# Performance work log

Hardware: AMD Instinct MI355X
Metric: run time of the kernel (lower is better)

## Reference

```python
import math
import jax, jax.numpy as jnp
import numpy as np

H = 16          # num_attention_heads
DH = 64         # attention_head_size
D = H * DH      # hidden_size
MAX_POS = 1024  # max_position_embeddings


def setup_inputs() -> dict:
    key = jax.random.key(0)
    ks = jax.random.split(key, 9)
    B, S = 8, 1024
    scale = 0.02
    return {
        "hidden_states": jax.random.normal(ks[0], (B, S, D), dtype=jnp.float32),
        "attention_mask": jnp.zeros((B, 1, 1, S), dtype=jnp.float32),
        "Wq": jax.random.normal(ks[1], (D, D), dtype=jnp.float32) * scale,
        "bq": jnp.zeros((D,), dtype=jnp.float32),
        "Wk": jax.random.normal(ks[2], (D, D), dtype=jnp.float32) * scale,
        "bk": jnp.zeros((D,), dtype=jnp.float32),
        "Wv": jax.random.normal(ks[3], (D, D), dtype=jnp.float32) * scale,
        "bv": jnp.zeros((D,), dtype=jnp.float32),
        "dist_emb": jax.random.normal(ks[4], (2 * MAX_POS - 1, DH), dtype=jnp.float32) * scale,
    }


def reference(hidden_states, attention_mask, Wq, bq, Wk, bk, Wv, bv, dist_emb):
    B, S, _ = hidden_states.shape
    # projections -> [B, H, S, DH]
    def heads(x):
        return x.reshape(B, S, H, DH).transpose(0, 2, 1, 3)
    q = heads(hidden_states @ Wq + bq)
    k = heads(hidden_states @ Wk + bk)
    v = heads(hidden_states @ Wv + bv)

    # fp32_cast_query_key == 'manual': cast q,k to fp32 before matmul (already fp32 here)
    scores = jnp.einsum("bhld,bhrd->bhlr", q.astype(jnp.float32), k.astype(jnp.float32))
    scores = scores / math.sqrt(DH)

    # relative_key_query positional bias
    pos = jnp.arange(S)
    distance = pos[:, None] - pos[None, :] + (MAX_POS - 1)   # [S, S]
    pe = dist_emb[distance].astype(q.dtype)                   # [S, S, DH]
    scores = scores + jnp.einsum("bhld,lrd->bhlr", q, pe) \
                     + jnp.einsum("bhrd,lrd->bhlr", k, pe)

    scores = scores + attention_mask
    # fp32_cast_attention_scores=True: softmax in fp32
    probs = jax.nn.softmax(scores.astype(jnp.float32), axis=-1).astype(hidden_states.dtype)

    ctx = jnp.einsum("bhlr,bhrd->bhld", probs, v)  # [B, H, S, DH]
    ctx = ctx.transpose(0, 2, 1, 3).reshape(B, S, D)
    return ctx
```

## Files before the change

kernel.cpp:

```cpp
#include <hip/hip_runtime.h>
#include <stdint.h>

typedef unsigned short u16;
typedef short bf16x8 __attribute__((ext_vector_type(8)));
typedef float f32x4 __attribute__((ext_vector_type(4)));
typedef u16 u16x8 __attribute__((ext_vector_type(8)));
typedef u16 u16x4 __attribute__((ext_vector_type(4)));

#define NB 8
#define NS 1024
#define NH 16
#define NDH 64
#define ND 1024

#define AS1 __attribute__((address_space(1)))
#define AS3 __attribute__((address_space(3)))

__device__ __forceinline__ int SWZ(int row, int colbyte){
  return (row << 7) + (colbyte ^ ((row & 7) << 4));
}

__device__ __forceinline__ u16 f2b(float x){
  unsigned u = __float_as_uint(x);
  u += 0x7FFFu + ((u >> 16) & 1u);
  return (u16)(u >> 16);
}
__device__ __forceinline__ float b2f(u16 h){ return __uint_as_float(((unsigned)h) << 16); }

__global__ void cast_f32_bf16(const float* __restrict__ in, u16* __restrict__ out, long n){
  long i = ((long)blockIdx.x * blockDim.x + threadIdx.x) * 8;
  if (i + 8 <= n){
    float4 a = *(const float4*)&in[i];
    float4 b = *(const float4*)&in[i + 4];
    u16x8 o;
    o[0]=f2b(a.x); o[1]=f2b(a.y); o[2]=f2b(a.z); o[3]=f2b(a.w);
    o[4]=f2b(b.x); o[5]=f2b(b.y); o[6]=f2b(b.z); o[7]=f2b(b.w);
    *(u16x8*)&out[i] = o;
  }
}

__global__ void transpose_w(const float* __restrict__ Wq, const float* __restrict__ Wk,
                            const float* __restrict__ Wv, u16* __restrict__ wt){
  __shared__ float tile[64][65];
  int p = blockIdx.z;
  const float* W = (p == 0) ? Wq : ((p == 1) ? Wk : Wv);
  int n0 = blockIdx.x * 64, k0 = blockIdx.y * 64;
  int t = threadIdx.x;
  int row = t >> 2, cb = (t & 3) * 16;
  #pragma unroll
  for (int cc = 0; cc < 4; ++cc){
    float4 v = *(const float4*)&W[(size_t)(k0 + row) * ND + n0 + cb + cc * 4];
    tile[row][cb + cc*4 + 0] = v.x; tile[row][cb + cc*4 + 1] = v.y;
    tile[row][cb + cc*4 + 2] = v.z; tile[row][cb + cc*4 + 3] = v.w;
  }
  __syncthreads();
  u16x8 o0, o1;
  #pragma unroll
  for (int kk = 0; kk < 8; ++kk) o0[kk] = f2b(tile[cb + kk][row]);
  #pragma unroll
  for (int kk = 0; kk < 8; ++kk) o1[kk] = f2b(tile[cb + 8 + kk][row]);
  size_t ob = ((size_t)(p * ND + n0 + row)) * ND + k0 + cb;
  *(u16x8*)&wt[ob]     = o0;
  *(u16x8*)&wt[ob + 8] = o1;
}

__global__ __launch_bounds__(256) void qkv_gemm(
    const u16* __restrict__ hsb, const u16* __restrict__ wtb,
    const float* __restrict__ bq, const float* __restrict__ bk, const float* __restrict__ bv,
    u16* __restrict__ qb, u16* __restrict__ kb, u16* __restrict__ vt){
  __shared__ __attribute__((aligned(16))) u16 Al[128 * 32];
  __shared__ __attribute__((aligned(16))) u16 Bl[128 * 32];
  int t = threadIdx.x;
  int lane = t & 63, w = t >> 6;
  int li = lane & 15, g = lane >> 4;
  int m0 = blockIdx.y * 128, n0 = blockIdx.x * 128;
  int wm = (w >> 1) * 64, wn = (w & 1) * 64;
  f32x4 acc[4][4];
  #pragma unroll
  for (int a = 0; a < 4; ++a)
    #pragma unroll
    for (int b = 0; b < 4; ++b){ f32x4 z = {0.f,0.f,0.f,0.f}; acc[a][b] = z; }

  for (int kt = 0; kt < 32; ++kt){
    __syncthreads();
    #pragma unroll
    for (int ph = 0; ph < 2; ++ph){
      int c = ph * 256 + t;
      int row = c >> 2, ch = c & 3;
      const u16* ga = &hsb[(size_t)(m0 + row) * ND + kt * 32 + ch * 8];
      __builtin_amdgcn_global_load_lds((const AS1 void*)ga,
          (AS3 void*)&Al[(ph * 256 + w * 64) * 8], 16, 0, 0);
      const u16* gb = &wtb[(size_t)(n0 + row) * ND + kt * 32 + ch * 8];
      __builtin_amdgcn_global_load_lds((const AS1 void*)gb,
          (AS3 void*)&Bl[(ph * 256 + w * 64) * 8], 16, 0, 0);
    }
    asm volatile("s_waitcnt vmcnt(0)" ::: "memory");
    __syncthreads();
    bf16x8 af[4], bfr[4];
    #pragma unroll
    for (int mt = 0; mt < 4; ++mt)
      af[mt] = *(const bf16x8*)&Al[(wm + mt * 16 + li) * 32 + g * 8];
    #pragma unroll
    for (int nt = 0; nt < 4; ++nt)
      bfr[nt] = *(const bf16x8*)&Bl[(wn + nt * 16 + li) * 32 + g * 8];
    #pragma unroll
    for (int mt = 0; mt < 4; ++mt)
      #pragma unroll
      for (int nt = 0; nt < 4; ++nt)
        acc[mt][nt] = __builtin_amdgcn_mfma_f32_16x16x32_bf16(af[mt], bfr[nt], acc[mt][nt], 0, 0, 0);
  }

  int proj = n0 >> 10;
  const float* bias = (proj == 0) ? bq : ((proj == 1) ? bk : bv);
  #pragma unroll
  for (int nt = 0; nt < 4; ++nt){
    int n = n0 + wn + nt * 16 + li;
    int nc = n & 1023;
    float bv_ = bias[nc];
    #pragma unroll
    for (int mt = 0; mt < 4; ++mt){
      #pragma unroll
      for (int r = 0; r < 4; ++r){
        int m = m0 + wm + mt * 16 + g * 4 + r;
        u16 hv = f2b(acc[mt][nt][r] + bv_);
        if (proj == 0)      qb[(size_t)m * ND + nc] = hv;
        else if (proj == 1) kb[(size_t)m * ND + nc] = hv;
        else {
          int bb = m >> 10, s = m & 1023;
          int hh = nc >> 6, dh = nc & 63;
          vt[((size_t)(bb * NH + hh) * NDH + dh) * NS + s] = hv;
        }
      }
    }
  }
}

__global__ __launch_bounds__(256, 3) void attn(
    const u16* __restrict__ qb, const u16* __restrict__ kb,
    const u16* __restrict__ vt, const u16* __restrict__ eb,
    const float* __restrict__ mask, float* __restrict__ out){
  __shared__ __attribute__((aligned(16))) u16 k_lds[64 * 72];
  __shared__ __attribute__((aligned(16))) u16 v_lds[64 * 72];
  __shared__ __attribute__((aligned(16))) u16 u2[128 * 64];
  __shared__ __attribute__((aligned(16))) u16 w2[128 * 64];

  int t = threadIdx.x, lane = t & 63, w = t >> 6;
  int li = lane & 15, g = lane >> 4;
  int lt = blockIdx.x, bh = blockIdx.y;
  int b = bh >> 4, h = bh & 15;
  int l0 = lt * 64;
  int iA  = w * 16 + g * 4;
  int iA2 = iA * 2;
  int li2 = li * 2;
  int ttc = iA + 63 - li;
  int colw = iA2;

  bf16x8 qf[2];
  {
    size_t qoff = ((size_t)(b * NS + l0 + w * 16 + li)) * ND + h * NDH;
    qf[0] = *(const bf16x8*)&qb[qoff + 0 + g * 8];
    qf[1] = *(const bf16x8*)&qb[qoff + 32 + g * 8];
  }

  bf16x8 ehi[4][2];
  #pragma unroll
  for (int nt = 0; nt < 4; ++nt){
    int er = l0 + 1024 + nt * 16 + li;
    if (er > 2046) er = 2046;
    #pragma unroll
    for (int k2 = 0; k2 < 2; ++k2)
      ehi[nt][k2] = *(const bf16x8*)&eb[(size_t)er * NDH + k2 * 32 + g * 8];
  }

  u16x8 rk[2], rv[2];
  {
    #pragma unroll
    for (int ph = 0; ph < 2; ++ph){
      int c = ph * 256 + t, row = c >> 3, ch = c & 7;
      rk[ph] = *(const u16x8*)&kb[((size_t)(b * NS + row)) * ND + h * NDH + ch * 8];
      rv[ph] = *(const u16x8*)&vt[((size_t)(bh * NDH + row)) * NS + ch * 8];
    }
  }

  f32x4 oacc[4];
  #pragma unroll
  for (int i = 0; i < 4; ++i){ f32x4 z = {0.f,0.f,0.f,0.f}; oacc[i] = z; }
  float mold[4] = {-1e30f, -1e30f, -1e30f, -1e30f};
  float lsum[4] = {0.f, 0.f, 0.f, 0.f};

  for (int kt2 = 0; kt2 < 16; ++kt2){
    int r0 = kt2 * 64;
    int ebase = l0 - r0 + 960;

    __syncthreads();
    #pragma unroll
    for (int ph = 0; ph < 2; ++ph){
      int c = ph * 256 + t, row = c >> 3, ch = c & 7;
      *(u16x8*)&k_lds[row * 72 + ch * 8] = rk[ph];
      *(u16x8*)&v_lds[row * 72 + ch * 8] = rv[ph];
    }
    __syncthreads();

    {
      int rn = ((kt2 + 1) & 15) * 64;
      #pragma unroll
      for (int ph = 0; ph < 2; ++ph){
        int c = ph * 256 + t, row = c >> 3, ch = c & 7;
        rk[ph] = *(const u16x8*)&kb[((size_t)(b * NS + rn + row)) * ND + h * NDH + ch * 8];
        rv[ph] = *(const u16x8*)&vt[((size_t)(bh * NDH + row)) * NS + rn + ch * 8];
      }
    }

    bf16x8 elo[4][2];
    #pragma unroll
    for (int nt = 0; nt < 4; ++nt){
      int er = ebase + nt * 16 + li;
      #pragma unroll
      for (int k2 = 0; k2 < 2; ++k2)
        elo[nt][k2] = *(const bf16x8*)&eb[(size_t)er * NDH + k2 * 32 + g * 8];
    }

    bf16x8 kf[2];
    kf[0] = *(const bf16x8*)&k_lds[(w * 16 + li) * 72 + 0 + g * 8];
    kf[1] = *(const bf16x8*)&k_lds[(w * 16 + li) * 72 + 32 + g * 8];

    f32x4 sacc[4];
    #pragma unroll
    for (int jt = 0; jt < 4; ++jt){
      f32x4 z = {0.f,0.f,0.f,0.f}; sacc[jt] = z;
      #pragma unroll
      for (int k2 = 0; k2 < 2; ++k2){
        bf16x8 kbf = *(const bf16x8*)&k_lds[(jt * 16 + li) * 72 + k2 * 32 + g * 8];
        sacc[jt] = __builtin_amdgcn_mfma_f32_16x16x32_bf16(qf[k2], kbf, sacc[jt], 0, 0, 0);
      }
    }

    #pragma unroll
    for (int nt = 4; nt < 8; ++nt){
      int trow = nt * 16 + li;
      f32x4 ua = {0.f,0.f,0.f,0.f}, wa = {0.f,0.f,0.f,0.f};
      #pragma unroll
      for (int k2 = 0; k2 < 2; ++k2){
        ua = __builtin_amdgcn_mfma_f32_16x16x32_bf16(qf[k2], ehi[nt - 4][k2], ua, 0, 0, 0);
        wa = __builtin_amdgcn_mfma_f32_16x16x32_bf16(kf[k2], ehi[nt - 4][k2], wa, 0, 0, 0);
      }
      u16x4 up, wp;
      #pragma unroll
      for (int r = 0; r < 4; ++r){ up[r] = f2b(ua[r]); wp[r] = f2b(wa[r]); }
      *(u16x4*)((char*)u2 + SWZ(trow, colw)) = up;
      *(u16x4*)((char*)w2 + SWZ(trow, colw)) = wp;
    }
    #pragma unroll
    for (int nt = 0; nt < 4; ++nt){
      int trow = nt * 16 + li;
      f32x4 ua = {0.f,0.f,0.f,0.f}, wa = {0.f,0.f,0.f,0.f};
      #pragma unroll
      for (int k2 = 0; k2 < 2; ++k2){
        ua = __builtin_amdgcn_mfma_f32_16x16x32_bf16(qf[k2], elo[nt][k2], ua, 0, 0, 0);
        wa = __builtin_amdgcn_mfma_f32_16x16x32_bf16(kf[k2], elo[nt][k2], wa, 0, 0, 0);
      }
      u16x4 up, wp;
      #pragma unroll
      for (int r = 0; r < 4; ++r){ up[r] = f2b(ua[r]); wp[r] = f2b(wa[r]); }
      *(u16x4*)((char*)u2 + SWZ(trow, colw)) = up;
      *(u16x4*)((char*)w2 + SWZ(trow, colw)) = wp;
    }
    #pragma unroll
    for (int nt = 0; nt < 4; ++nt){
      ehi[nt][0] = elo[nt][0];
      ehi[nt][1] = elo[nt][1];
    }
    __syncthreads();

    float sv[4][4];
    #pragma unroll
    for (int jt = 0; jt < 4; ++jt){
      float mk = mask[b * NS + r0 + jt * 16 + li];
      int j2 = jt * 32 + li2;
      #pragma unroll
      for (int r = 0; r < 4; ++r){
        int tt = ttc + r - jt * 16;
        int byU = (tt << 7) + ((iA2 + 2 * r) ^ ((tt & 7) << 4));
        int byW = (tt << 7) + (j2 ^ ((tt & 7) << 4));
        float u  = b2f(*(const u16*)((const char*)u2 + byU));
        float ww = b2f(*(const u16*)((const char*)w2 + byW));
        sv[jt][r] = sacc[jt][r] * 0.125f + u + ww + mk;
      }
    }

    float rmax[4], rsum[4];
    #pragma unroll
    for (int r = 0; r < 4; ++r)
      rmax[r] = fmaxf(fmaxf(sv[0][r], sv[1][r]), fmaxf(sv[2][r], sv[3][r]));
    #pragma unroll
    for (int xm = 1; xm <= 8; xm <<= 1)
      #pragma unroll
      for (int r = 0; r < 4; ++r)
        rmax[r] = fmaxf(rmax[r], __shfl_xor(rmax[r], xm));
    float mnew[4], fac[4];
    #pragma unroll
    for (int r = 0; r < 4; ++r){
      mnew[r] = fmaxf(mold[r], rmax[r]);
      fac[r]  = __expf(mold[r] - mnew[r]);
    }
    float pr[4][4];
    #pragma unroll
    for (int r = 0; r < 4; ++r) rsum[r] = 0.f;
    #pragma unroll
    for (int jt = 0; jt < 4; ++jt)
      #pragma unroll
      for (int r = 0; r < 4; ++r){
        pr[jt][r] = __expf(sv[jt][r] - mnew[r]);
        rsum[r] += pr[jt][r];
      }
    #pragma unroll
    for (int xm = 1; xm <= 8; xm <<= 1)
      #pragma unroll
      for (int r = 0; r < 4; ++r)
        rsum[r] += __shfl_xor(rsum[r], xm);
    #pragma unroll
    for (int r = 0; r < 4; ++r){
      lsum[r] = lsum[r] * fac[r] + rsum[r];
      mold[r] = mnew[r];
    }
    #pragma unroll
    for (int nt2 = 0; nt2 < 4; ++nt2)
      #pragma unroll
      for (int r = 0; r < 4; ++r)
        oacc[nt2][r] *= fac[r];

    __syncthreads();
    #pragma unroll
    for (int jt = 0; jt < 4; ++jt)
      #pragma unroll
      for (int r = 0; r < 4; ++r){
        int prow = w * 16 + g * 4 + r;
        *(u16*)((char*)u2 + SWZ(prow, jt * 32 + li2)) = f2b(pr[jt][r]);
      }

    #pragma unroll
    for (int k2 = 0; k2 < 2; ++k2){
      bf16x8 pf = *(const bf16x8*)((const char*)u2 + SWZ(w * 16 + li, k2 * 64 + g * 16));
      #pragma unroll
      for (int nt2 = 0; nt2 < 4; ++nt2){
        bf16x8 vf = *(const bf16x8*)&v_lds[(nt2 * 16 + li) * 72 + k2 * 32 + g * 8];
        oacc[nt2] = __builtin_amdgcn_mfma_f32_16x16x32_bf16(pf, vf, oacc[nt2], 0, 0, 0);
      }
    }
  }

  #pragma unroll
  for (int nt2 = 0; nt2 < 4; ++nt2)
    #pragma unroll
    for (int r = 0; r < 4; ++r){
      int row = l0 + w * 16 + g * 4 + r;
      out[((size_t)(b * NS + row)) * ND + h * NDH + nt2 * 16 + li] = oacc[nt2][r] / lsum[r];
    }
}

extern "C" void kernel_launch(void* const* d_in, const int* in_sizes, int n_in,
                              void* d_out, int out_size, void* d_ws, size_t ws_size,
                              hipStream_t stream){
  (void)in_sizes; (void)n_in; (void)out_size; (void)ws_size;
  const float* hs   = (const float*)d_in[0];
  const float* mask = (const float*)d_in[1];
  const float* Wq   = (const float*)d_in[2];
  const float* bq   = (const float*)d_in[3];
  const float* Wk   = (const float*)d_in[4];
  const float* bk   = (const float*)d_in[5];
  const float* Wv   = (const float*)d_in[6];
  const float* bv   = (const float*)d_in[7];
  const float* de   = (const float*)d_in[8];
  float* out = (float*)d_out;
  char* ws = (char*)d_ws;

  u16* hsb = (u16*)(ws);
  u16* wtb = (u16*)(ws + 16777216);
  u16* eb  = (u16*)(ws + 23068672);
  u16* qb  = (u16*)(ws + 23330816);
  u16* kb  = (u16*)(ws + 40108032);
  u16* vt  = (u16*)(ws + 56885248);

  cast_f32_bf16<<<4096, 256, 0, stream>>>(hs, hsb, 8388608L);
  cast_f32_bf16<<<64, 256, 0, stream>>>(de, eb, 131008L);
  transpose_w<<<dim3(16, 16, 3), 256, 0, stream>>>(Wq, Wk, Wv, wtb);
  qkv_gemm<<<dim3(24, 64), 256, 0, stream>>>(hsb, wtb, bq, bk, bv, qb, kb, vt);
  attn<<<dim3(16, 128), 256, 0, stream>>>(qb, kb, vt, eb, mask, out);
}
```

Baseline: 458.7 us.

## Reuse Q-position products across key tiles via ring buffer and raise MFMA priority

The Q·E positional term for the upper 64 relative-distance rows carries over from one key tile to the next. It is now kept in a 128-row circular LDS buffer indexed by ebase mod 128 and computed only on the first tile, which removes half of the Q-side positional MFMAs. The softmax probabilities are staged in the w2 buffer so that u2 survives across iterations. s_setprio is raised around the MFMA sections to favour matrix issue across waves. The ring indexing adds address arithmetic, and correctness depends on the carried rows matching exactly under the modulo wrap.

```diff
diff --git a/kernel.cpp b/kernel.cpp
--- a/kernel.cpp
+++ b/kernel.cpp
@@ -191,6 +191,7 @@
   for (int kt2 = 0; kt2 < 16; ++kt2){
     int r0 = kt2 * 64;
     int ebase = l0 - r0 + 960;
+    int s0 = ebase & 127;
 
     __syncthreads();
     #pragma unroll
@@ -224,6 +225,7 @@
     kf[0] = *(const bf16x8*)&k_lds[(w * 16 + li) * 72 + 0 + g * 8];
     kf[1] = *(const bf16x8*)&k_lds[(w * 16 + li) * 72 + 32 + g * 8];
 
+    __builtin_amdgcn_s_setprio(1);
     f32x4 sacc[4];
     #pragma unroll
     for (int jt = 0; jt < 4; ++jt){
@@ -238,17 +240,25 @@
     #pragma unroll
     for (int nt = 4; nt < 8; ++nt){
       int trow = nt * 16 + li;
-      f32x4 ua = {0.f,0.f,0.f,0.f}, wa = {0.f,0.f,0.f,0.f};
-      #pragma unroll
-      for (int k2 = 0; k2 < 2; ++k2){
-        ua = __builtin_amdgcn_mfma_f32_16x16x32_bf16(qf[k2], ehi[nt - 4][k2], ua, 0, 0, 0);
+      f32x4 wa = {0.f,0.f,0.f,0.f};
+      #pragma unroll
+      for (int k2 = 0; k2 < 2; ++k2)
         wa = __builtin_amdgcn_mfma_f32_16x16x32_bf16(kf[k2], ehi[nt - 4][k2], wa, 0, 0, 0);
-      }
-      u16x4 up, wp;
-      #pragma unroll
-      for (int r = 0; r < 4; ++r){ up[r] = f2b(ua[r]); wp[r] = f2b(wa[r]); }
-      *(u16x4*)((char*)u2 + SWZ(trow, colw)) = up;
+      u16x4 wp;
+      #pragma unroll
+      for (int r = 0; r < 4; ++r) wp[r] = f2b(wa[r]);
       *(u16x4*)((char*)w2 + SWZ(trow, colw)) = wp;
+      if (kt2 == 0){
+        f32x4 ua = {0.f,0.f,0.f,0.f};
+        #pragma unroll
+        for (int k2 = 0; k2 < 2; ++k2)
+          ua = __builtin_amdgcn_mfma_f32_16x16x32_bf16(qf[k2], ehi[nt - 4][k2], ua, 0, 0, 0);
+        int su = (s0 + trow) & 127;
+        u16x4 up;
+        #pragma unroll
+        for (int r = 0; r < 4; ++r) up[r] = f2b(ua[r]);
+        *(u16x4*)((char*)u2 + SWZ(su, colw)) = up;
+      }
     }
     #pragma unroll
     for (int nt = 0; nt < 4; ++nt){
@@ -259,12 +269,15 @@
         ua = __builtin_amdgcn_mfma_f32_16x16x32_bf16(qf[k2], elo[nt][k2], ua, 0, 0, 0);
         wa = __builtin_amdgcn_mfma_f32_16x16x32_bf16(kf[k2], elo[nt][k2], wa, 0, 0, 0);
       }
+      int su = (s0 + trow) & 127;
       u16x4 up, wp;
       #pragma unroll
       for (int r = 0; r < 4; ++r){ up[r] = f2b(ua[r]); wp[r] = f2b(wa[r]); }
-      *(u16x4*)((char*)u2 + SWZ(trow, colw)) = up;
+      *(u16x4*)((char*)u2 + SWZ(su, colw)) = up;
       *(u16x4*)((char*)w2 + SWZ(trow, colw)) = wp;
     }
+    __builtin_amdgcn_s_setprio(0);
+
     #pragma unroll
     for (int nt = 0; nt < 4; ++nt){
       ehi[nt][0] = elo[nt][0];
@@ -280,7 +293,8 @@
       #pragma unroll
       for (int r = 0; r < 4; ++r){
         int tt = ttc + r - jt * 16;
-        int byU = (tt << 7) + ((iA2 + 2 * r) ^ ((tt & 7) << 4));
+        int su = (s0 + tt) & 127;
+        int byU = (su << 7) + ((iA2 + 2 * r) ^ ((su & 7) << 4));
         int byW = (tt << 7) + (j2 ^ ((tt & 7) << 4));
         float u  = b2f(*(const u16*)((const char*)u2 + byU));
         float ww = b2f(*(const u16*)((const char*)w2 + byW));
@@ -335,18 +349,20 @@
       #pragma unroll
       for (int r = 0; r < 4; ++r){
         int prow = w * 16 + g * 4 + r;
-        *(u16*)((char*)u2 + SWZ(prow, jt * 32 + li2)) = f2b(pr[jt][r]);
-      }
-
+        *(u16*)((char*)w2 + SWZ(prow, jt * 32 + li2)) = f2b(pr[jt][r]);
+      }
+
+    __builtin_amdgcn_s_setprio(1);
     #pragma unroll
     for (int k2 = 0; k2 < 2; ++k2){
-      bf16x8 pf = *(const bf16x8*)((const char*)u2 + SWZ(w * 16 + li, k2 * 64 + g * 16));
+      bf16x8 pf = *(const bf16x8*)((const char*)w2 + SWZ(w * 16 + li, k2 * 64 + g * 16));
       #pragma unroll
       for (int nt2 = 0; nt2 < 4; ++nt2){
         bf16x8 vf = *(const bf16x8*)&v_lds[(nt2 * 16 + li) * 72 + k2 * 32 + g * 8];
         oacc[nt2] = __builtin_amdgcn_mfma_f32_16x16x32_bf16(pf, vf, oacc[nt2], 0, 0, 0);
       }
     }
+    __builtin_amdgcn_s_setprio(0);
   }
 
   #pragma unroll
```

After: 1.016 ms. 122% more time.
